# Optimization experiments

Measured on AMD Instinct MI355X. Metric: run time of the kernel, lower is better.

## Reference

```python
import jax, jax.numpy as jnp
import numpy as np

L = 32        # label_num = len(label2idx)
SOS = 0       # label2idx['[SOS]']
END = 1       # label2idx['[END]']
NEG = -10000.0
B, T = 512, 1024


def setup_inputs() -> dict:
    key = jax.random.key(0)
    k1, k2, k3 = jax.random.split(key, 3)
    emission = jax.random.normal(k1, (B, T, L), dtype=jnp.float32)
    label_ids = jax.random.randint(k2, (B, T), 0, L)
    transitions = jax.random.normal(k3, (L, L), dtype=jnp.float32)
    # CrfLayer.__init__: forbid transitions into [SOS] and out of [END]
    transitions = transitions.at[SOS, :].set(NEG).at[:, END].set(NEG)
    return {"emission": emission, "label_ids": label_ids, "transitions": transitions}


def reference(emission, label_ids, transitions):
    b, t, l = emission.shape
    # ---- _forward_alg: log-partition via sequential logsumexp recurrence ----
    alpha0 = jnp.full((b, l), NEG, dtype=emission.dtype).at[:, SOS].set(0.0)
    feats_t = jnp.transpose(emission, (1, 0, 2))  # [T, B, L]

    def step(alpha, feat):
        # aa[b, j, i] = alpha[b, i] + feat[b, j] + transitions[j, i]
        aa = alpha[:, None, :] + feat[:, :, None] + transitions[None, :, :]
        return jax.nn.logsumexp(aa, axis=2), None

    alpha, _ = jax.lax.scan(step, alpha0, feats_t)
    forward_score = jax.nn.logsumexp(alpha + transitions[END][None, :], axis=1)  # [B]

    # ---- _score_sentence: score of the gold path ----
    tags = jnp.concatenate(
        [jnp.full((b, 1), SOS, dtype=label_ids.dtype), label_ids], axis=1)  # [B, T+1]
    trans_score = transitions[tags[:, 1:], tags[:, :-1]].sum(axis=1)          # [B]
    emit_score = jnp.take_along_axis(
        emission, tags[:, 1:, None].astype(jnp.int32), axis=2)[..., 0].sum(axis=1)  # [B]
    gold_score = trans_score + emit_score + transitions[END, tags[:, -1]]

    # loss = sum(forward_score - gold_score)
    return jnp.sum(forward_score - gold_score)
```

## Files before the change

### kernel.cpp

```cpp
#include <hip/hip_runtime.h>


typedef float  f32x16 __attribute__((ext_vector_type(16)));
typedef short  s16x8  __attribute__((ext_vector_type(8)));
typedef float  f32x2  __attribute__((ext_vector_type(2)));

#define TT 1024
#define LL 32
#define BB 512
#define NW 16
#define CL 64
#define NCH 8
#define MS 33

union Frag { s16x8 v; unsigned u[4]; };

__device__ __forceinline__ unsigned pack_bf16(float lo, float hi) {
    return __builtin_amdgcn_perm(__float_as_uint(hi), __float_as_uint(lo), 0x07060302u);
}

__device__ __forceinline__ void skew_sleep(int n) {
    switch (n & 3) {
        case 1: __builtin_amdgcn_s_sleep(1); break;
        case 2: __builtin_amdgcn_s_sleep(2); break;
        case 3: __builtin_amdgcn_s_sleep(3); break;
        default: break;
    }
}

__global__ __launch_bounds__(NW * 64, 8) void crf_fused_kernel(
    const float* __restrict__ emission,
    const int*   __restrict__ label_ids,
    const float* __restrict__ transitions,
    float*       __restrict__ out)
{
    __shared__ __align__(16) float shM[NCH][32 * MS];
    __shared__ float shQ[2][64];
    __shared__ float tgArr[NW];
    __shared__ int   capArr[NW];

    const int tid  = threadIdx.x;
    const int w    = tid >> 6;
    const int lane = tid & 63;
    const int j    = lane & 31;
    const int h    = lane >> 5;
    const int b    = blockIdx.x;
    const int t0   = w * CL;

    const int*   labB = label_ids + b * TT + t0;
    const float* emB  = emission + ((size_t)b * TT + t0) * LL + j;

    {
        float g = 0.0f;
        int tt = t0 + lane;
        int l1 = labB[lane];
        int l0 = (tt == 0) ? 0 : label_ids[b * TT + tt - 1];
        g += transitions[(l1 << 5) + l0];
        g += emission[((size_t)b * TT + tt) * LL + l1];
        if (tt == TT - 1) g += transitions[32 + l1];
#pragma unroll
        for (int m = 32; m >= 1; m >>= 1) g += __shfl_xor(g, m, 64);
        if (lane == 0) tgArr[w] = g;
    }

    const float* trow = transitions + j * 32;
    f32x2 E0v[4], E1v[4];
#pragma unroll
    for (int p = 0; p < 4; ++p) {
        int c0 = ((2 * p) & 3)     + 8 * ((2 * p) >> 2)     + 4 * h;
        int c1 = ((2 * p + 1) & 3) + 8 * ((2 * p + 1) >> 2) + 4 * h;
        E0v[p][0] = __expf(trow[c0]);      E0v[p][1] = __expf(trow[c1]);
        E1v[p][0] = __expf(trow[16 + c0]); E1v[p][1] = __expf(trow[16 + c1]);
    }

    Frag B0, B1;
#pragma unroll
    for (int i = 0; i < 8; ++i) {
        int row = (i & 3) + 8 * (i >> 2) + 4 * h;
        B0.v[i] = (short)((row == j)      ? 0x3F80 : 0);
        B1.v[i] = (short)((row + 16 == j) ? 0x3F80 : 0);
    }

    f32x16 zc, acc;
#pragma unroll
    for (int i = 0; i < 16; ++i) zc[i] = 0.0f;

    float ring[8];
#pragma unroll
    for (int s = 0; s < 8; ++s) ring[s] = emB[s * LL];

    float sc = 1.0f;
    int   Cap = 0, elast = 0;

    skew_sleep((w >> 2) + ((blockIdx.x & 1) << 1));

    auto step = [&](int k, int s, bool refill) {
        float feat = ring[k];
        float fs = ((k & 3) == 0) ? (__expf(feat) * sc) : __expf(feat);
        f32x2 fs2; fs2[0] = fs; fs2[1] = fs;

        Frag A0, A1;
#pragma unroll
        for (int p = 0; p < 4; ++p) {
            f32x2 a = fs2 * E0v[p];
            f32x2 c = fs2 * E1v[p];
            A0.u[p] = pack_bf16(a[0], a[1]);
            A1.u[p] = pack_bf16(c[0], c[1]);
        }

        acc = __builtin_amdgcn_mfma_f32_32x32x16_bf16(A0.v, B0.v, zc, 0, 0, 0);
        acc = __builtin_amdgcn_mfma_f32_32x32x16_bf16(A1.v, B1.v, acc, 0, 0, 0);

        if ((k & 3) == 3) {
            int pb = __builtin_amdgcn_readlane(__float_as_int(acc[2]), 0);
            int e  = ((pb >> 23) & 0xff) - 127;
            sc = __int_as_float((127 - e) << 23);
            Cap += e;
            elast = e;
        }

        if (refill) ring[k] = emB[(s + 8) * LL];

#pragma unroll
        for (int p = 0; p < 4; ++p) {
            B0.u[p] = pack_bf16(acc[2 * p],     acc[2 * p + 1]);
            B1.u[p] = pack_bf16(acc[8 + 2 * p], acc[9 + 2 * p]);
        }
    };

    for (int s0 = 0; s0 < CL - 8; s0 += 8) {
#pragma unroll
        for (int k = 0; k < 8; ++k) step(k, s0 + k, true);
    }
#pragma unroll
    for (int k = 0; k < 8; ++k) step(k, CL - 8 + k, false);

    Cap -= elast;

    if (lane == 0) capArr[w] = Cap;

    if (w < NCH) {
#pragma unroll
        for (int r = 0; r < 16; ++r) {
            int row = (r & 3) + 8 * (r >> 2) + 4 * h;
            shM[w][row * MS + j] = acc[r];
        }
    }

    const float Eend = __expf(transitions[32 + j]);
    float q    = (j == 0) ? 1.0f : 0.0f;
    int   Cq   = 0;
    float gold = 0.0f;

    auto combine8 = [&](int base) {
#pragma unroll
        for (int c = 0; c < NCH; ++c) {
            shQ[c & 1][lane] = q;
            asm volatile("s_waitcnt lgkmcnt(0)" ::: "memory");
            __builtin_amdgcn_wave_barrier();
            const float* Mrow = &shM[c][j * MS];
            const float* qv   = &shQ[c & 1][h * 32];
            float a0 = 0.f, a1 = 0.f, a2 = 0.f, a3 = 0.f;
#pragma unroll
            for (int i = 0; i < 32; i += 4) {
                a0 = fmaf(Mrow[i],     qv[i],     a0);
                a1 = fmaf(Mrow[i + 1], qv[i + 1], a1);
                a2 = fmaf(Mrow[i + 2], qv[i + 2], a2);
                a3 = fmaf(Mrow[i + 3], qv[i + 3], a3);
            }
            float qn = (a0 + a1) + (a2 + a3);
            int pb = __builtin_amdgcn_readlane(__float_as_int(qn), 2);
            int e  = ((pb >> 23) & 0xff) - 127;
            qn *= __int_as_float((127 - e) << 23);
            Cq += e + capArr[base + c];
            gold += tgArr[base + c];
            q = qn;
        }
    };

    __syncthreads();

    if (w == 0) combine8(0);

    __syncthreads();

    if (w >= NCH) {
#pragma unroll
        for (int r = 0; r < 16; ++r) {
            int row = (r & 3) + 8 * (r >> 2) + 4 * h;
            shM[w - NCH][row * MS + j] = acc[r];
        }
    }

    __syncthreads();

    if (w == 0) {
        combine8(NCH);

        float v = q * Eend;
#pragma unroll
        for (int m = 16; m >= 1; m >>= 1) v += __shfl_xor(v, m, 32);
        float fwd = __logf(v) + (float)Cq * 0.69314718055994531f;

        if (lane == 0) atomicAdd(out, fwd - gold);
    }
}

extern "C" void kernel_launch(void* const* d_in, const int* in_sizes, int n_in,
                              void* d_out, int out_size, void* d_ws, size_t ws_size,
                              hipStream_t stream)
{
    const float* emission    = (const float*)d_in[0];
    const int*   label_ids   = (const int*)d_in[1];
    const float* transitions = (const float*)d_in[2];
    float* out = (float*)d_out;

    (void)hipMemsetAsync(out, 0, sizeof(float), stream);
    crf_fused_kernel<<<BB, NW * 64, 0, stream>>>(emission, label_ids, transitions, out);
}
```

Before: 146.9 us.

## Give each wave two interleaved time chunks to overlap independent MFMA chains

Halves the waves per block from 16 to 8, and each wave now runs two independent 64-step chunk recurrences in interleaved fashion, with separate accumulators, rings and scale state. The goal is to hide MFMA and pack latency within the serial dependency chain through instruction-level parallelism rather than relying on more waves. In exchange it uses more registers per wave, lowers the occupancy hint to 4, and reduces wave-level parallelism. Gold-score accumulation moves to the end of the combine step.

```diff
diff --git a/kernel.cpp b/kernel.cpp
--- a/kernel.cpp
+++ b/kernel.cpp
@@ -8,7 +8,7 @@
 #define TT 1024
 #define LL 32
 #define BB 512
-#define NW 16
+#define NW 8
 #define CL 64
 #define NCH 8
 #define MS 33
@@ -28,7 +28,7 @@
     }
 }
 
-__global__ __launch_bounds__(NW * 64, 8) void crf_fused_kernel(
+__global__ __launch_bounds__(NW * 64, 4) void crf_fused_kernel(
     const float* __restrict__ emission,
     const int*   __restrict__ label_ids,
     const float* __restrict__ transitions,
@@ -37,7 +37,7 @@
     __shared__ __align__(16) float shM[NCH][32 * MS];
     __shared__ float shQ[2][64];
     __shared__ float tgArr[NW];
-    __shared__ int   capArr[NW];
+    __shared__ int   capArr[2 * NW];
 
     const int tid  = threadIdx.x;
     const int w    = tid >> 6;
@@ -45,19 +45,20 @@
     const int j    = lane & 31;
     const int h    = lane >> 5;
     const int b    = blockIdx.x;
-    const int t0   = w * CL;
-
-    const int*   labB = label_ids + b * TT + t0;
-    const float* emB  = emission + ((size_t)b * TT + t0) * LL + j;
+    const int t0   = w * (2 * CL);
 
     {
+        const int* labB = label_ids + b * TT + t0;
         float g = 0.0f;
-        int tt = t0 + lane;
-        int l1 = labB[lane];
-        int l0 = (tt == 0) ? 0 : label_ids[b * TT + tt - 1];
-        g += transitions[(l1 << 5) + l0];
-        g += emission[((size_t)b * TT + tt) * LL + l1];
-        if (tt == TT - 1) g += transitions[32 + l1];
+#pragma unroll
+        for (int u = 0; u < 2; ++u) {
+            int tt = t0 + 64 * u + lane;
+            int l1 = labB[64 * u + lane];
+            int l0 = (tt == 0) ? 0 : label_ids[b * TT + tt - 1];
+            g += transitions[(l1 << 5) + l0];
+            g += emission[((size_t)b * TT + tt) * LL + l1];
+            if (tt == TT - 1) g += transitions[32 + l1];
+        }
 #pragma unroll
         for (int m = 32; m >= 1; m >>= 1) g += __shfl_xor(g, m, 64);
         if (lane == 0) tgArr[w] = g;
@@ -73,28 +74,34 @@
         E1v[p][0] = __expf(trow[16 + c0]); E1v[p][1] = __expf(trow[16 + c1]);
     }
 
-    Frag B0, B1;
+    Frag B0a, B1a, B0b, B1b;
 #pragma unroll
     for (int i = 0; i < 8; ++i) {
         int row = (i & 3) + 8 * (i >> 2) + 4 * h;
-        B0.v[i] = (short)((row == j)      ? 0x3F80 : 0);
-        B1.v[i] = (short)((row + 16 == j) ? 0x3F80 : 0);
-    }
-
-    f32x16 zc, acc;
+        short lo = (short)((row == j)      ? 0x3F80 : 0);
+        short hi = (short)((row + 16 == j) ? 0x3F80 : 0);
+        B0a.v[i] = lo;  B1a.v[i] = hi;
+        B0b.v[i] = lo;  B1b.v[i] = hi;
+    }
+
+    f32x16 zc, accA, accB;
 #pragma unroll
     for (int i = 0; i < 16; ++i) zc[i] = 0.0f;
 
-    float ring[8];
-#pragma unroll
-    for (int s = 0; s < 8; ++s) ring[s] = emB[s * LL];
-
-    float sc = 1.0f;
-    int   Cap = 0, elast = 0;
-
-    skew_sleep((w >> 2) + ((blockIdx.x & 1) << 1));
-
-    auto step = [&](int k, int s, bool refill) {
+    const float* emA = emission + ((size_t)b * TT + t0) * LL + j;
+    const float* emBp = emA + (size_t)CL * LL;
+
+    float ringA[8], ringB[8];
+#pragma unroll
+    for (int s = 0; s < 8; ++s) { ringA[s] = emA[s * LL]; ringB[s] = emBp[s * LL]; }
+
+    float scA = 1.0f, scB = 1.0f;
+    int   CapA = 0, elA = 0, CapB = 0, elB = 0;
+
+    skew_sleep(w + ((blockIdx.x & 1) << 1));
+
+    auto step = [&](Frag& B0, Frag& B1, f32x16& acc, auto& ring, float& sc,
+                    int& Cap, int& elast, const float* em, int k, int s, bool refill) {
         float feat = ring[k];
         float fs = ((k & 3) == 0) ? (__expf(feat) * sc) : __expf(feat);
         f32x2 fs2; fs2[0] = fs; fs2[1] = fs;
@@ -119,7 +126,7 @@
             elast = e;
         }
 
-        if (refill) ring[k] = emB[(s + 8) * LL];
+        if (refill) ring[k] = em[(s + 8) * LL];
 
 #pragma unroll
         for (int p = 0; p < 4; ++p) {
@@ -130,27 +137,33 @@
 
     for (int s0 = 0; s0 < CL - 8; s0 += 8) {
 #pragma unroll
-        for (int k = 0; k < 8; ++k) step(k, s0 + k, true);
-    }
-#pragma unroll
-    for (int k = 0; k < 8; ++k) step(k, CL - 8 + k, false);
-
-    Cap -= elast;
-
-    if (lane == 0) capArr[w] = Cap;
-
-    if (w < NCH) {
+        for (int k = 0; k < 8; ++k) {
+            step(B0a, B1a, accA, ringA, scA, CapA, elA, emA,  k, s0 + k, true);
+            step(B0b, B1b, accB, ringB, scB, CapB, elB, emBp, k, s0 + k, true);
+        }
+    }
+#pragma unroll
+    for (int k = 0; k < 8; ++k) {
+        step(B0a, B1a, accA, ringA, scA, CapA, elA, emA,  k, CL - 8 + k, false);
+        step(B0b, B1b, accB, ringB, scB, CapB, elB, emBp, k, CL - 8 + k, false);
+    }
+
+    CapA -= elA;
+    CapB -= elB;
+    if (lane == 0) { capArr[2 * w] = CapA; capArr[2 * w + 1] = CapB; }
+
+    if (w < 4) {
 #pragma unroll
         for (int r = 0; r < 16; ++r) {
             int row = (r & 3) + 8 * (r >> 2) + 4 * h;
-            shM[w][row * MS + j] = acc[r];
+            shM[2 * w][row * MS + j]     = accA[r];
+            shM[2 * w + 1][row * MS + j] = accB[r];
         }
     }
 
     const float Eend = __expf(transitions[32 + j]);
-    float q    = (j == 0) ? 1.0f : 0.0f;
-    int   Cq   = 0;
-    float gold = 0.0f;
+    float q  = (j == 0) ? 1.0f : 0.0f;
+    int   Cq = 0;
 
     auto combine8 = [&](int base) {
 #pragma unroll
@@ -173,7 +186,6 @@
             int e  = ((pb >> 23) & 0xff) - 127;
             qn *= __int_as_float((127 - e) << 23);
             Cq += e + capArr[base + c];
-            gold += tgArr[base + c];
             q = qn;
         }
     };
@@ -184,11 +196,12 @@
 
     __syncthreads();
 
-    if (w >= NCH) {
+    if (w >= 4) {
 #pragma unroll
         for (int r = 0; r < 16; ++r) {
             int row = (r & 3) + 8 * (r >> 2) + 4 * h;
-            shM[w - NCH][row * MS + j] = acc[r];
+            shM[2 * (w - 4)][row * MS + j]     = accA[r];
+            shM[2 * (w - 4) + 1][row * MS + j] = accB[r];
         }
     }
 
@@ -196,6 +209,10 @@
 
     if (w == 0) {
         combine8(NCH);
+
+        float gold = 0.0f;
+#pragma unroll
+        for (int c = 0; c < NW; ++c) gold += tgArr[c];
 
         float v = q * Eend;
 #pragma unroll
```

Result: faster. 139.3 us (-5.2%).
